# Kernel optimization log

Measured on AMD Instinct MI355X. Metric: run time of the kernel, lower is better.

## Reference

```python
import jax, jax.numpy as jnp
import numpy as np

HEADS = 4
ATTN_DIM = 32
SCALE = ATTN_DIM ** -0.5
EPS = 1e-12  # F.normalize eps


def rmsnorm_chan(x, g):
    # x: (b, c, h, w); RMSNorm over channel dim: F.normalize(x, dim=1) * g * sqrt(c)
    c = x.shape[1]
    n = jnp.sqrt(jnp.sum(x * x, axis=1, keepdims=True))
    return x / jnp.maximum(n, EPS) * g[None, :, None, None] * jnp.sqrt(jnp.asarray(c, x.dtype))


def setup_inputs() -> dict:
    key = jax.random.key(0)
    ks = jax.random.split(key, 4)
    b, c, h, w = 16, 256, 64, 64
    hidden = HEADS * ATTN_DIM  # 128
    x = jax.random.normal(ks[0], (b, c, h, w), dtype=jnp.float32)
    norm_g = jnp.ones((c,), jnp.float32)
    w_qkv = jax.random.normal(ks[1], (3 * hidden, c), dtype=jnp.float32) * 0.02
    mem_kv = jax.random.normal(ks[2], (2, HEADS, ATTN_DIM, 4), dtype=jnp.float32)
    w_out = jax.random.normal(ks[3], (c, hidden), dtype=jnp.float32) * 0.02
    b_out = jnp.zeros((c,), jnp.float32)
    out_norm_g = jnp.ones((c,), jnp.float32)
    return {"x": x, "norm_g": norm_g, "w_qkv": w_qkv, "mem_kv": mem_kv,
            "w_out": w_out, "b_out": b_out, "out_norm_g": out_norm_g}


def reference(x, norm_g, w_qkv, mem_kv, w_out, b_out, out_norm_g):
    b, c, h, w = x.shape
    n = h * w
    xn = rmsnorm_chan(x, norm_g).reshape(b, c, n)  # pre-norm, flatten spatial
    # 1x1 conv (no bias) == channel matmul: (b, 3*hidden, n)
    qkv = jnp.einsum('oc,bcn->bon', w_qkv, xn)
    q, k, v = jnp.split(qkv, 3, axis=1)
    # (b, heads, d, n)
    q = q.reshape(b, HEADS, ATTN_DIM, n)
    k = k.reshape(b, HEADS, ATTN_DIM, n)
    v = v.reshape(b, HEADS, ATTN_DIM, n)
    # prepend memory kv (broadcast over batch): (b, heads, d, num_mem + n)
    mk = jnp.broadcast_to(mem_kv[0][None], (b, HEADS, ATTN_DIM, mem_kv.shape[-1]))
    mv = jnp.broadcast_to(mem_kv[1][None], (b, HEADS, ATTN_DIM, mem_kv.shape[-1]))
    k = jnp.concatenate([mk, k], axis=-1)
    v = jnp.concatenate([mv, v], axis=-1)
    q = jax.nn.softmax(q, axis=-2) * SCALE  # softmax over feature dim d
    k = jax.nn.softmax(k, axis=-1)          # softmax over token dim n
    context = jnp.einsum('bhdn,bhen->bhde', k, v)   # small d x e per head
    out = jnp.einsum('bhde,bhdn->bhen', context, q)  # (b, heads, e, n)
    out = out.reshape(b, HEADS * ATTN_DIM, h, w)
    # 1x1 conv with bias, then RMSNorm
    out = jnp.einsum('oc,bchw->bohw', w_out, out) + b_out[None, :, None, None]
    return rmsnorm_chan(out, out_norm_g)
```

## Files before the change

kernel.cpp:

```cpp
#include <hip/hip_runtime.h>
#include <hip/hip_bf16.h>

typedef __hip_bfloat16 bf16;
typedef __attribute__((ext_vector_type(8))) short bf16x8;
typedef __attribute__((ext_vector_type(4))) float floatx4;

#define NB 16
#define NC 256
#define NPIX 4096
#define NHID 128
#define NH 4
#define ND 32
#define NMEM 4
#define QSCALE 0.17677669529663687f

__device__ __forceinline__ void dma16(const void* g, void* l){
  __builtin_amdgcn_global_load_lds(
      (const __attribute__((address_space(1))) unsigned int*)g,
      (__attribute__((address_space(3))) unsigned int*)l, 16, 0, 0);
}

__global__ void k0_zero(float* __restrict__ p, int n){
  int i = blockIdx.x*256 + threadIdx.x;
  if (i < n) p[i] = 0.f;
}

__launch_bounds__(256)
__global__ void kW(const float* __restrict__ wqkv, const float* __restrict__ g,
                   bf16* __restrict__ wgpack){
  const int u = blockIdx.x*256 + threadIdx.x;
  const int s = u / 1536;
  const int r = u - s*1536;
  const int tile = r >> 6, l = r & 63;
  const int row = tile*16 + (l & 15);
  const int kb  = s*32 + (l >> 4)*8;
  const float* wp = wqkv + (size_t)row*NC + kb;
  floatx4 w0 = *(const floatx4*)wp;
  floatx4 w1 = *(const floatx4*)(wp + 4);
  floatx4 g0 = *(const floatx4*)(g + kb);
  floatx4 g1 = *(const floatx4*)(g + kb + 4);
  alignas(16) bf16 tmp[8];
  #pragma unroll
  for (int i = 0; i < 4; ++i){
    tmp[i]   = __float2bfloat16(w0[i]*g0[i]);
    tmp[4+i] = __float2bfloat16(w1[i]*g1[i]);
  }
  *(uint4*)(wgpack + (size_t)u*8) = *(const uint4*)tmp;
}

__launch_bounds__(256)
__global__ void kA(const float* __restrict__ x, const bf16* __restrict__ wgpack,
                   float* __restrict__ dout,
                   float* __restrict__ ctxu, float* __restrict__ zacc){
  __shared__ char smem alignas(16) [60672];
  bf16 (*Pb)[72] = (bf16(*)[72])smem;
  bf16 (*Vb)[72] = (bf16(*)[72])(smem + 18432);
  float* ssqL = (float*)(smem + 59392);
  float* sL   = (float*)(smem + 60416);
  const int t = threadIdx.x;
  const int pb = blockIdx.x * 64, b = blockIdx.y;
  const int wv = t >> 6, lane = t & 63, m = lane & 15, q4 = lane >> 4;
  const int px_st = t & 63, cg_st = t >> 6;
  const float* xb = x + (size_t)b*NC*NPIX;
  float ssq = 0.f;

  auto stage = [&](int s, int buf){
    const bf16* gt = wgpack + ((size_t)(s*24 + wv*6)*64 + lane)*8;
    char* lt = smem + buf*24576 + wv*6144;
    #pragma unroll
    for (int tt = 0; tt < 6; ++tt)
      dma16(gt + tt*512, lt + tt*1024);
    const float* xp = xb + (size_t)(s*32 + cg_st*8)*NPIX + pb + px_st;
    alignas(16) bf16 tmp[8];
    #pragma unroll
    for (int j = 0; j < 8; ++j){
      float v = xp[(size_t)j*NPIX];
      ssq += v*v;
      tmp[j] = __float2bfloat16(v);
    }
    bf16 (*Xb)[40] = (bf16(*)[40])(smem + 49152 + buf*5120);
    *(uint4*)&Xb[px_st][cg_st*8] = *(const uint4*)tmp;
  };

  stage(0, 0);
  __syncthreads();
  floatx4 acc[6][4] = {};
  for (int s = 0; s < 8; ++s){
    const int buf = s & 1;
    if (s < 7) stage(s + 1, buf ^ 1);
    bf16 (*Xb)[40] = (bf16(*)[40])(smem + 49152 + buf*5120);
    const bf16* Ab = (const bf16*)(smem + buf*24576);
    bf16x8 bfr[4];
    #pragma unroll
    for (int pt = 0; pt < 4; ++pt)
      bfr[pt] = *(const bf16x8*)&Xb[pt*16 + m][q4*8];
    #pragma unroll
    for (int rt = 0; rt < 6; ++rt){
      bf16x8 af = *(const bf16x8*)(Ab + (size_t)wv*3072 + rt*512 + (q4*16 + m)*8);
      #pragma unroll
      for (int pt = 0; pt < 4; ++pt)
        acc[rt][pt] = __builtin_amdgcn_mfma_f32_16x16x32_bf16(af, bfr[pt], acc[rt][pt], 0, 0, 0);
    }
    __syncthreads();
  }
  ssqL[cg_st*64 + px_st] = ssq;
  __syncthreads();
  if (t < 64){
    float tot = ssqL[t] + ssqL[64 + t] + ssqL[128 + t] + ssqL[192 + t];
    sL[t] = 16.0f / fmaxf(sqrtf(tot), 1e-12f);
  }
  __syncthreads();
  float sv[4];
  #pragma unroll
  for (int pt = 0; pt < 4; ++pt) sv[pt] = sL[pt*16 + m];
  #pragma unroll
  for (int pr = 0; pr < 3; ++pr){
    const int ra = 2*pr, rb = 2*pr + 1;
    const int row0 = wv*96 + pr*32;
    const int type = row0 >> 7;
    if (type == 0){
      const int slice = row0 >> 5;
      const int j0 = (q4 & 1)*4;
      #pragma unroll
      for (int pt = 0; pt < 4; ++pt){
        float va[4], vb[4];
        float mx = -1e30f;
        #pragma unroll
        for (int r = 0; r < 4; ++r){
          va[r] = acc[ra][pt][r]*sv[pt];
          vb[r] = acc[rb][pt][r]*sv[pt];
          mx = fmaxf(mx, fmaxf(va[r], vb[r]));
        }
        mx = fmaxf(mx, __shfl_xor(mx, 16, 64));
        mx = fmaxf(mx, __shfl_xor(mx, 32, 64));
        float se = 0.f;
        #pragma unroll
        for (int r = 0; r < 4; ++r){
          va[r] = __expf(va[r] - mx); vb[r] = __expf(vb[r] - mx);
          se += va[r] + vb[r];
        }
        se += __shfl_xor(se, 16, 64);
        se += __shfl_xor(se, 32, 64);
        const float inv = QSCALE / se;
        alignas(8) bf16 pka[4], pkb[4];
        #pragma unroll
        for (int r = 0; r < 4; ++r){
          pka[r] = __float2bfloat16(va[r]*inv);
          pkb[r] = __float2bfloat16(vb[r]*inv);
        }
        const int ca = (slice*4 + pt)*4 + (q4 >> 1);
        const int cb = ca + 2;
        bf16* pa = (bf16*)(dout + (size_t)(b*NC + ca)*NPIX + pb) + m*8 + j0;
        bf16* pv = (bf16*)(dout + (size_t)(b*NC + cb)*NPIX + pb) + m*8 + j0;
        *(uint2*)pa = *(const uint2*)pka;
        *(uint2*)pv = *(const uint2*)pkb;
      }
    } else if (type == 1){
      const int d0 = row0 - 128;
      float za[4] = {}, zb[4] = {};
      #pragma unroll
      for (int pt = 0; pt < 4; ++pt){
        #pragma unroll
        for (int r = 0; r < 4; ++r){
          float pa = __expf(acc[ra][pt][r]*sv[pt]);
          float pv = __expf(acc[rb][pt][r]*sv[pt]);
          za[r] += pa; zb[r] += pv;
          Pb[d0      + q4*4 + r][pt*16 + m] = __float2bfloat16(pa);
          Pb[d0 + 16 + q4*4 + r][pt*16 + m] = __float2bfloat16(pv);
        }
      }
      #pragma unroll
      for (int r = 0; r < 4; ++r){
        #pragma unroll
        for (int o = 1; o < 16; o <<= 1){
          za[r] += __shfl_xor(za[r], o, 64);
          zb[r] += __shfl_xor(zb[r], o, 64);
        }
      }
      if (m == 0){
        #pragma unroll
        for (int r = 0; r < 4; ++r){
          atomicAdd(&zacc[b*NHID + d0      + q4*4 + r], za[r]);
          atomicAdd(&zacc[b*NHID + d0 + 16 + q4*4 + r], zb[r]);
        }
      }
    } else {
      const int v0 = row0 - 256;
      #pragma unroll
      for (int pt = 0; pt < 4; ++pt)
        #pragma unroll
        for (int r = 0; r < 4; ++r){
          Vb[v0      + q4*4 + r][pt*16 + m] = __float2bfloat16(acc[ra][pt][r]*sv[pt]);
          Vb[v0 + 16 + q4*4 + r][pt*16 + m] = __float2bfloat16(acc[rb][pt][r]*sv[pt]);
        }
    }
  }
  __syncthreads();
  floatx4 cx[2][2] = {};
  #pragma unroll
  for (int k0t = 0; k0t < 64; k0t += 32){
    bf16x8 af[2], bf[2];
    #pragma unroll
    for (int dt = 0; dt < 2; ++dt) af[dt] = *(const bf16x8*)&Pb[wv*32 + dt*16 + m][k0t + q4*8];
    #pragma unroll
    for (int et = 0; et < 2; ++et) bf[et] = *(const bf16x8*)&Vb[wv*32 + et*16 + m][k0t + q4*8];
    #pragma unroll
    for (int dt = 0; dt < 2; ++dt)
      #pragma unroll
      for (int et = 0; et < 2; ++et)
        cx[dt][et] = __builtin_amdgcn_mfma_f32_16x16x32_bf16(af[dt], bf[et], cx[dt][et], 0, 0, 0);
  }
  float* cb2 = ctxu + (size_t)(b*NH + wv)*ND*ND;
  #pragma unroll
  for (int dt = 0; dt < 2; ++dt)
    #pragma unroll
    for (int et = 0; et < 2; ++et)
      #pragma unroll
      for (int r = 0; r < 4; ++r)
        atomicAdd(&cb2[(dt*16 + q4*4 + r)*ND + et*16 + m], cx[dt][et][r]);
}

__launch_bounds__(256)
__global__ void k4_weff(const float* __restrict__ ctxu, const float* __restrict__ zacc,
                        const float* __restrict__ memkv, const float* __restrict__ wout,
                        bf16* __restrict__ wpack){
  const int idx = blockIdx.x*256 + threadIdx.x;
  const int b   = idx >> 15;
  const int o   = (idx >> 7) & 255;
  const int hd  = idx & 127;
  const int h = hd >> 5, d = hd & 31;
  const float* mk = memkv + hd*NMEM;
  float me[4];
  float z = zacc[b*NHID + hd];
  #pragma unroll
  for (int j = 0; j < 4; ++j){ me[j] = __expf(mk[j]); z += me[j]; }
  const float invz = 1.0f / z;
  const float* cp = ctxu + (size_t)((b*NH + h)*ND + d)*ND;
  const float* wp = wout + (size_t)o*NHID + h*ND;
  const float* mv = memkv + (size_t)(NHID + h*ND)*NMEM;
  float acc = 0.f;
  #pragma unroll
  for (int e = 0; e < ND; ++e){
    float ce = cp[e];
    #pragma unroll
    for (int j = 0; j < 4; ++j) ce += me[j]*mv[e*NMEM + j];
    acc += ce*wp[e];
  }
  const int slice = hd >> 5, q4k = (hd >> 3) & 3, j = hd & 7;
  const int tile = o >> 4, m16 = o & 15;
  wpack[((size_t)((b*4 + slice)*16 + tile)*64 + q4k*16 + m16)*8 + j] = __float2bfloat16(acc*invz);
}

__launch_bounds__(256)
__global__ void k5_out(float* dout, const bf16* __restrict__ wpack,
                       const float* __restrict__ bout, const float* __restrict__ gout){
  __shared__ char smem alignas(16) [50432];
  bf16* Qb = (bf16*)(smem + 32768);
  float* red = (float*)(smem + 49152);
  float* nf  = (float*)(smem + 50176);
  const int t = threadIdx.x;
  const int pb = blockIdx.x * 64, b = blockIdx.y;
  const int wv = t >> 6, lane = t & 63, m = lane & 15, q4 = lane >> 4;
  {
    #pragma unroll
    for (int i = 0; i < 4; ++i){
      const int tau = wv*4 + i;
      const char* gq = (const char*)(dout + (size_t)(b*NC + tau*4 + q4)*NPIX + pb) + m*16;
      dma16(gq, smem + 32768 + tau*1024);
    }
  }
  {
    const bf16* gt = wpack + ((size_t)((b*4)*16 + wv*4)*64 + lane)*8;
    char* lt = smem + wv*4096;
    #pragma unroll
    for (int tt = 0; tt < 4; ++tt) dma16(gt + tt*512, lt + tt*1024);
  }
  __syncthreads();
  floatx4 acc[4][4] = {};
  for (int s = 0; s < 4; ++s){
    const int buf = s & 1;
    if (s < 3){
      const bf16* gt = wpack + ((size_t)((b*4 + s+1)*16 + wv*4)*64 + lane)*8;
      char* lt = smem + (buf^1)*16384 + wv*4096;
      #pragma unroll
      for (int tt = 0; tt < 4; ++tt) dma16(gt + tt*512, lt + tt*1024);
    }
    const bf16* Wb = (const bf16*)(smem + buf*16384);
    bf16x8 bfr[4], af[4];
    #pragma unroll
    for (int pt = 0; pt < 4; ++pt)
      bfr[pt] = *(const bf16x8*)(Qb + (size_t)(s*4 + pt)*512 + (q4*16 + m)*8);
    #pragma unroll
    for (int rt = 0; rt < 4; ++rt)
      af[rt] = *(const bf16x8*)(Wb + (size_t)(wv*4 + rt)*512 + (q4*16 + m)*8);
    #pragma unroll
    for (int rt = 0; rt < 4; ++rt)
      #pragma unroll
      for (int pt = 0; pt < 4; ++pt)
        acc[rt][pt] = __builtin_amdgcn_mfma_f32_16x16x32_bf16(af[rt], bfr[pt], acc[rt][pt], 0, 0, 0);
    __syncthreads();
  }
  float ps[4] = {0.f, 0.f, 0.f, 0.f};
  #pragma unroll
  for (int rt = 0; rt < 4; ++rt){
    const int row = wv*64 + rt*16 + q4*4;
    #pragma unroll
    for (int r = 0; r < 4; ++r){
      const float bias = bout[row + r];
      #pragma unroll
      for (int pt = 0; pt < 4; ++pt){
        acc[rt][pt][r] += bias;
        ps[pt] += acc[rt][pt][r]*acc[rt][pt][r];
      }
    }
  }
  #pragma unroll
  for (int pt = 0; pt < 4; ++pt){
    ps[pt] += __shfl_xor(ps[pt], 16, 64);
    ps[pt] += __shfl_xor(ps[pt], 32, 64);
  }
  if (q4 == 0){
    #pragma unroll
    for (int pt = 0; pt < 4; ++pt) red[wv*64 + pt*16 + m] = ps[pt];
  }
  __syncthreads();
  if (t < 64){
    float tot = red[t] + red[64 + t] + red[128 + t] + red[192 + t];
    nf[t] = 16.0f / fmaxf(sqrtf(tot), 1e-12f);
  }
  __syncthreads();
  float nv[4];
  #pragma unroll
  for (int pt = 0; pt < 4; ++pt) nv[pt] = nf[pt*16 + m];
  #pragma unroll
  for (int rt = 0; rt < 4; ++rt){
    const int row = wv*64 + rt*16 + q4*4;
    #pragma unroll
    for (int r = 0; r < 4; ++r){
      const float gg = gout[row + r];
      float* op = dout + (size_t)(b*NC + row + r)*NPIX + pb + m;
      #pragma unroll
      for (int pt = 0; pt < 4; ++pt)
        op[pt*16] = acc[rt][pt][r]*nv[pt]*gg;
    }
  }
}

extern "C" void kernel_launch(void* const* d_in, const int* in_sizes, int n_in,
                              void* d_out, int out_size, void* d_ws, size_t ws_size,
                              hipStream_t stream) {
  (void)in_sizes; (void)n_in; (void)out_size; (void)ws_size;
  const float* x     = (const float*)d_in[0];
  const float* ng    = (const float*)d_in[1];
  const float* wqkv  = (const float*)d_in[2];
  const float* memkv = (const float*)d_in[3];
  const float* wout  = (const float*)d_in[4];
  const float* bout  = (const float*)d_in[5];
  const float* gout  = (const float*)d_in[6];
  float* dout = (float*)d_out;
  char* ws = (char*)d_ws;
  bf16*  wgpack = (bf16*)(ws);
  bf16*  wpack  = (bf16*)(ws + 196608);
  float* ctxu   = (float*)(ws + 1245184);
  float* zacc   = (float*)(ws + 1507328);

  k0_zero<<<dim3(264),     256, 0, stream>>>(ctxu, 65536 + 2048);
  kW     <<<dim3(48),      256, 0, stream>>>(wqkv, ng, wgpack);
  kA     <<<dim3(64, 16),  256, 0, stream>>>(x, wgpack, dout, ctxu, zacc);
  k4_weff<<<dim3(2048),    256, 0, stream>>>(ctxu, zacc, memkv, wout, wpack);
  k5_out <<<dim3(64, 16),  256, 0, stream>>>(dout, wpack, bout, gout);
}
```

Before: 188.3 us.

## Pipeline x loads two stages ahead, retile weff in LDS, fold zeroing into kW

The QKV kernel now prefetches x two channel-slices ahead into registers and overlaps the LDS DMA with MFMA work, using explicit waitcnt and barrier placement instead of __syncthreads. The weff kernel is restructured so each block caches the context matrices and a w_out tile in shared memory and writes packed bf16 vectors, replacing per-element redundant global reads. The zeroing kernel is folded into kW to save a launch. k5 drops its per-stage block barriers, since each wave only reads its own LDS region. The hand-placed waitcnts raise the risk of ordering bugs.

```diff
diff --git a/kernel.cpp b/kernel.cpp
--- a/kernel.cpp
+++ b/kernel.cpp
@@ -14,21 +14,21 @@
 #define NMEM 4
 #define QSCALE 0.17677669529663687f
 
+#define VMCNT(n) asm volatile("s_waitcnt vmcnt(" #n ")" ::: "memory")
+#define LGKM0()  asm volatile("s_waitcnt lgkmcnt(0)" ::: "memory")
+#define SCHEDB() __builtin_amdgcn_sched_barrier(0)
+
 __device__ __forceinline__ void dma16(const void* g, void* l){
   __builtin_amdgcn_global_load_lds(
       (const __attribute__((address_space(1))) unsigned int*)g,
       (__attribute__((address_space(3))) unsigned int*)l, 16, 0, 0);
 }
 
-__global__ void k0_zero(float* __restrict__ p, int n){
-  int i = blockIdx.x*256 + threadIdx.x;
-  if (i < n) p[i] = 0.f;
-}
-
 __launch_bounds__(256)
 __global__ void kW(const float* __restrict__ wqkv, const float* __restrict__ g,
-                   bf16* __restrict__ wgpack){
+                   bf16* __restrict__ wgpack, float* __restrict__ zbase){
   const int u = blockIdx.x*256 + threadIdx.x;
+  for (int z = u; z < 65536 + 2048; z += 48*256) zbase[z] = 0.f;
   const int s = u / 1536;
   const int r = u - s*1536;
   const int tile = r >> 6, l = r & 63;
@@ -63,45 +63,69 @@
   const int px_st = t & 63, cg_st = t >> 6;
   const float* xb = x + (size_t)b*NC*NPIX;
   float ssq = 0.f;
-
-  auto stage = [&](int s, int buf){
-    const bf16* gt = wgpack + ((size_t)(s*24 + wv*6)*64 + lane)*8;
-    char* lt = smem + buf*24576 + wv*6144;
-    #pragma unroll
-    for (int tt = 0; tt < 6; ++tt)
-      dma16(gt + tt*512, lt + tt*1024);
-    const float* xp = xb + (size_t)(s*32 + cg_st*8)*NPIX + pb + px_st;
+  float xr[2][8];
+
+  auto xissue = [&](int c, float* dst){
+    const float* xp = xb + (size_t)(c*32 + cg_st*8)*NPIX + pb + px_st;
+    #pragma unroll
+    for (int j = 0; j < 8; ++j) dst[j] = xp[(size_t)j*NPIX];
+  };
+  auto xwrite = [&](int c, const float* v){
     alignas(16) bf16 tmp[8];
     #pragma unroll
     for (int j = 0; j < 8; ++j){
-      float v = xp[(size_t)j*NPIX];
-      ssq += v*v;
-      tmp[j] = __float2bfloat16(v);
-    }
-    bf16 (*Xb)[40] = (bf16(*)[40])(smem + 49152 + buf*5120);
+      ssq += v[j]*v[j];
+      tmp[j] = __float2bfloat16(v[j]);
+    }
+    bf16 (*Xb)[40] = (bf16(*)[40])(smem + 49152 + (c&1)*5120);
     *(uint4*)&Xb[px_st][cg_st*8] = *(const uint4*)tmp;
   };
-
-  stage(0, 0);
-  __syncthreads();
+  auto dmaw = [&](int c){
+    const bf16* gt = wgpack + ((size_t)(c*24 + wv*6)*64 + lane)*8;
+    char* lt = smem + (c&1)*24576 + wv*6144;
+    #pragma unroll
+    for (int tt = 0; tt < 6; ++tt) dma16(gt + tt*512, lt + tt*1024);
+  };
+
+  xissue(0, xr[0]);
+  SCHEDB();
+  dmaw(0);
+  SCHEDB();
+  xissue(1, xr[1]);
+  SCHEDB();
+  xwrite(0, xr[0]);
+  LGKM0();
+  VMCNT(8);
+  __builtin_amdgcn_s_barrier();
+  SCHEDB();
+
   floatx4 acc[6][4] = {};
+  #pragma unroll
   for (int s = 0; s < 8; ++s){
     const int buf = s & 1;
-    if (s < 7) stage(s + 1, buf ^ 1);
     bf16 (*Xb)[40] = (bf16(*)[40])(smem + 49152 + buf*5120);
     const bf16* Ab = (const bf16*)(smem + buf*24576);
-    bf16x8 bfr[4];
+    bf16x8 bfr[4], af[6];
     #pragma unroll
     for (int pt = 0; pt < 4; ++pt)
       bfr[pt] = *(const bf16x8*)&Xb[pt*16 + m][q4*8];
     #pragma unroll
-    for (int rt = 0; rt < 6; ++rt){
-      bf16x8 af = *(const bf16x8*)(Ab + (size_t)wv*3072 + rt*512 + (q4*16 + m)*8);
+    for (int rt = 0; rt < 6; ++rt)
+      af[rt] = *(const bf16x8*)(Ab + (size_t)wv*3072 + rt*512 + (q4*16 + m)*8);
+    if (s < 7) dmaw(s + 1);
+    SCHEDB();
+    if (s < 6) xissue(s + 2, xr[buf]);
+    SCHEDB();
+    #pragma unroll
+    for (int rt = 0; rt < 6; ++rt)
       #pragma unroll
       for (int pt = 0; pt < 4; ++pt)
-        acc[rt][pt] = __builtin_amdgcn_mfma_f32_16x16x32_bf16(af, bfr[pt], acc[rt][pt], 0, 0, 0);
-    }
-    __syncthreads();
+        acc[rt][pt] = __builtin_amdgcn_mfma_f32_16x16x32_bf16(af[rt], bfr[pt], acc[rt][pt], 0, 0, 0);
+    if (s < 7) xwrite(s + 1, xr[buf ^ 1]);
+    LGKM0();
+    if (s < 6) { VMCNT(8); } else { VMCNT(0); }
+    __builtin_amdgcn_s_barrier();
+    SCHEDB();
   }
   ssqL[cg_st*64 + px_st] = ssq;
   __syncthreads();
@@ -199,16 +223,16 @@
   floatx4 cx[2][2] = {};
   #pragma unroll
   for (int k0t = 0; k0t < 64; k0t += 32){
-    bf16x8 af[2], bf[2];
-    #pragma unroll
-    for (int dt = 0; dt < 2; ++dt) af[dt] = *(const bf16x8*)&Pb[wv*32 + dt*16 + m][k0t + q4*8];
-    #pragma unroll
-    for (int et = 0; et < 2; ++et) bf[et] = *(const bf16x8*)&Vb[wv*32 + et*16 + m][k0t + q4*8];
+    bf16x8 af2[2], bf2[2];
+    #pragma unroll
+    for (int dt = 0; dt < 2; ++dt) af2[dt] = *(const bf16x8*)&Pb[wv*32 + dt*16 + m][k0t + q4*8];
+    #pragma unroll
+    for (int et = 0; et < 2; ++et) bf2[et] = *(const bf16x8*)&Vb[wv*32 + et*16 + m][k0t + q4*8];
     #pragma unroll
     for (int dt = 0; dt < 2; ++dt)
       #pragma unroll
       for (int et = 0; et < 2; ++et)
-        cx[dt][et] = __builtin_amdgcn_mfma_f32_16x16x32_bf16(af[dt], bf[et], cx[dt][et], 0, 0, 0);
+        cx[dt][et] = __builtin_amdgcn_mfma_f32_16x16x32_bf16(af2[dt], bf2[et], cx[dt][et], 0, 0, 0);
   }
   float* cb2 = ctxu + (size_t)(b*NH + wv)*ND*ND;
   #pragma unroll
@@ -224,31 +248,52 @@
 __global__ void k4_weff(const float* __restrict__ ctxu, const float* __restrict__ zacc,
                         const float* __restrict__ memkv, const float* __restrict__ wout,
                         bf16* __restrict__ wpack){
-  const int idx = blockIdx.x*256 + threadIdx.x;
-  const int b   = idx >> 15;
-  const int o   = (idx >> 7) & 255;
-  const int hd  = idx & 127;
-  const int h = hd >> 5, d = hd & 31;
-  const float* mk = memkv + hd*NMEM;
-  float me[4];
-  float z = zacc[b*NHID + hd];
-  #pragma unroll
-  for (int j = 0; j < 4; ++j){ me[j] = __expf(mk[j]); z += me[j]; }
-  const float invz = 1.0f / z;
-  const float* cp = ctxu + (size_t)((b*NH + h)*ND + d)*ND;
-  const float* wp = wout + (size_t)o*NHID + h*ND;
-  const float* mv = memkv + (size_t)(NHID + h*ND)*NMEM;
-  float acc = 0.f;
-  #pragma unroll
-  for (int e = 0; e < ND; ++e){
-    float ce = cp[e];
-    #pragma unroll
-    for (int j = 0; j < 4; ++j) ce += me[j]*mv[e*NMEM + j];
-    acc += ce*wp[e];
-  }
-  const int slice = hd >> 5, q4k = (hd >> 3) & 3, j = hd & 7;
-  const int tile = o >> 4, m16 = o & 15;
-  wpack[((size_t)((b*4 + slice)*16 + tile)*64 + q4k*16 + m16)*8 + j] = __float2bfloat16(acc*invz);
+  __shared__ float ctxL[4][32][32];
+  __shared__ float woutL[64][129];
+  const int t = threadIdx.x;
+  const int o0 = blockIdx.x * 64, b = blockIdx.y;
+  {
+    const float* ws = wout + (size_t)o0*NHID;
+    #pragma unroll
+    for (int i = 0; i < 32; ++i){
+      const int idx = i*256 + t;
+      woutL[idx >> 7][idx & 127] = ws[idx];
+    }
+  }
+  if (t < 128){
+    const int h = t >> 5;
+    const float* mk = memkv + t*NMEM;
+    float me[4]; float z = zacc[b*NHID + t];
+    #pragma unroll
+    for (int j = 0; j < 4; ++j){ me[j] = __expf(mk[j]); z += me[j]; }
+    const float invz = 1.0f / z;
+    const float* cp = ctxu + (size_t)(b*NH*ND + t)*ND;
+    const float* mv = memkv + (size_t)(NHID + h*ND)*NMEM;
+    #pragma unroll
+    for (int e = 0; e < ND; ++e){
+      float ce = cp[e];
+      #pragma unroll
+      for (int j = 0; j < 4; ++j) ce += me[j]*mv[e*NMEM + j];
+      ctxL[h][t & 31][e] = ce * invz;
+    }
+  }
+  __syncthreads();
+  const int ol = t & 63, g = t >> 6;
+  float out[32] = {};
+  #pragma unroll
+  for (int e = 0; e < 32; ++e){
+    const float we = woutL[ol][g*32 + e];
+    #pragma unroll
+    for (int d = 0; d < 32; ++d) out[d] += ctxL[g][d][e] * we;
+  }
+  const int o = o0 + ol, tile = o >> 4, m16 = o & 15;
+  #pragma unroll
+  for (int q4k = 0; q4k < 4; ++q4k){
+    alignas(16) bf16 tmp[8];
+    #pragma unroll
+    for (int j = 0; j < 8; ++j) tmp[j] = __float2bfloat16(out[q4k*8 + j]);
+    *(uint4*)(wpack + ((size_t)((b*4 + g)*16 + tile)*64 + q4k*16 + m16)*8) = *(const uint4*)tmp;
+  }
 }
 
 __launch_bounds__(256)
@@ -275,30 +320,35 @@
     #pragma unroll
     for (int tt = 0; tt < 4; ++tt) dma16(gt + tt*512, lt + tt*1024);
   }
-  __syncthreads();
+  VMCNT(0);
+  __builtin_amdgcn_s_barrier();
+  SCHEDB();
   floatx4 acc[4][4] = {};
+  #pragma unroll
   for (int s = 0; s < 4; ++s){
     const int buf = s & 1;
+    const bf16* Wb = (const bf16*)(smem + buf*16384);
+    bf16x8 bfr[4], af[4];
+    #pragma unroll
+    for (int pt = 0; pt < 4; ++pt)
+      bfr[pt] = *(const bf16x8*)(Qb + (size_t)(s*4 + pt)*512 + (q4*16 + m)*8);
+    #pragma unroll
+    for (int rt = 0; rt < 4; ++rt)
+      af[rt] = *(const bf16x8*)(Wb + (size_t)(wv*4 + rt)*512 + (q4*16 + m)*8);
     if (s < 3){
       const bf16* gt = wpack + ((size_t)((b*4 + s+1)*16 + wv*4)*64 + lane)*8;
       char* lt = smem + (buf^1)*16384 + wv*4096;
       #pragma unroll
       for (int tt = 0; tt < 4; ++tt) dma16(gt + tt*512, lt + tt*1024);
     }
-    const bf16* Wb = (const bf16*)(smem + buf*16384);
-    bf16x8 bfr[4], af[4];
-    #pragma unroll
-    for (int pt = 0; pt < 4; ++pt)
-      bfr[pt] = *(const bf16x8*)(Qb + (size_t)(s*4 + pt)*512 + (q4*16 + m)*8);
-    #pragma unroll
-    for (int rt = 0; rt < 4; ++rt)
-      af[rt] = *(const bf16x8*)(Wb + (size_t)(wv*4 + rt)*512 + (q4*16 + m)*8);
+    SCHEDB();
     #pragma unroll
     for (int rt = 0; rt < 4; ++rt)
       #pragma unroll
       for (int pt = 0; pt < 4; ++pt)
         acc[rt][pt] = __builtin_amdgcn_mfma_f32_16x16x32_bf16(af[rt], bfr[pt], acc[rt][pt], 0, 0, 0);
-    __syncthreads();
+    if (s < 3) { VMCNT(0); }
+    SCHEDB();
   }
   float ps[4] = {0.f, 0.f, 0.f, 0.f};
   #pragma unroll
@@ -364,9 +414,8 @@
   float* ctxu   = (float*)(ws + 1245184);
   float* zacc   = (float*)(ws + 1507328);
 
-  k0_zero<<<dim3(264),     256, 0, stream>>>(ctxu, 65536 + 2048);
-  kW     <<<dim3(48),      256, 0, stream>>>(wqkv, ng, wgpack);
+  kW     <<<dim3(48),      256, 0, stream>>>(wqkv, ng, wgpack, ctxu);
   kA     <<<dim3(64, 16),  256, 0, stream>>>(x, wgpack, dout, ctxu, zacc);
-  k4_weff<<<dim3(2048),    256, 0, stream>>>(ctxu, zacc, memkv, wout, wpack);
+  k4_weff<<<dim3(4, 16),   256, 0, stream>>>(ctxu, zacc, memkv, wout, wpack);
   k5_out <<<dim3(64, 16),  256, 0, stream>>>(dout, wpack, bout, gout);
 }
```

Result: faster. 178.6 us (-5.1%).
